# Optimization experiments

Hardware: AMD Instinct MI355X
Metric: run time of the kernel (lower is better)

The kernel has to match this reference:

```python
import jax, jax.numpy as jnp
import numpy as np

NB = 4          # batch size (len(unique(batch_ixs)))
NA = 1048576    # anchors per batch element
C_FG = 2        # foreground classes (probs has C_FG+1 columns)
K = 6000        # pre-NMS top-k, hard-coded in source
PATCH = (256, 256, 128)


def setup_inputs():
    key = jax.random.key(0)
    k1, k2, k3 = jax.random.split(key, 3)
    H, W, D = PATCH
    scale = jnp.array([H, W, H, W, D, D], jnp.float32)
    anchors = jax.random.uniform(k1, (NA, 6), jnp.float32) * scale   # (y1,x1,y2,x2,z1,z2) in pixel coords
    probs = jax.nn.softmax(jax.random.normal(k2, (NB * NA, C_FG + 1), jnp.float32), axis=-1)
    deltas = jax.random.normal(k3, (NB * NA, 6), jnp.float32) * 0.1
    batch_ixs = jnp.repeat(jnp.arange(NB, dtype=jnp.int32), NA)
    return {"anchors": anchors, "probs": probs, "deltas": deltas, "batch_ixs": batch_ixs}


def _refine(anchors, probs, deltas, batch_ixs):
    H, W, D = PATCH
    scale = jnp.array([H, W, H, W, D, D], jnp.float32)
    std = jnp.array([0.1, 0.1, 0.1, 0.2, 0.2, 0.2], jnp.float32)
    anchors_rep = jnp.tile(anchors, (NB, 1))            # anchors.repeat(len(unique(batch_ixs)), 1)
    fg = probs[:, 1:]                                   # (N, C_FG)
    # flat descending sort + [:6000]  ==  top_k over the flat view
    top_s, top_i = jax.lax.top_k(fg.reshape(-1), K)
    prop = top_i // C_FG                                # proposal index
    cls = top_i % C_FG + 1                              # pred class id (1-based)
    b_ix = batch_ixs[prop]
    anc = jnp.floor(anchors_rep[prop] / scale)          # torch.div(..., rounding_mode='floor')
    dlt = deltas[prop] * std
    # apply_box_deltas_3D
    h = anc[:, 2] - anc[:, 0]
    w = anc[:, 3] - anc[:, 1]
    d = anc[:, 5] - anc[:, 4]
    cy = anc[:, 0] + 0.5 * h + dlt[:, 0] * h
    cx = anc[:, 1] + 0.5 * w + dlt[:, 1] * w
    cz = anc[:, 4] + 0.5 * d + dlt[:, 2] * d
    h = h * jnp.exp(dlt[:, 3])
    w = w * jnp.exp(dlt[:, 4])
    d = d * jnp.exp(dlt[:, 5])
    y1 = cy - 0.5 * h
    x1 = cx - 0.5 * w
    z1 = cz - 0.5 * d
    boxes = jnp.stack([y1, x1, y1 + h, x1 + w, z1, z1 + d], axis=1) * scale
    hi = jnp.array([H, W, H, W, D, D], jnp.float32)
    rois = jnp.round(jnp.clip(boxes, 0.0, hi))          # clip_to_window + round -> pre_nms_rois

    # per-(batch, class) selection, replicating the source's `order[order[:2]]` double indexing
    def select(b, c):
        mask = (b_ix == b) & (cls == c)
        lp = (jnp.cumsum(mask) - 1).astype(jnp.int32)   # local position within class subset (valid where mask)
        ms = jnp.where(mask, top_s, -jnp.inf)
        ord_full = jnp.argsort(-ms)                     # local rank r -> global candidate index
        order_arr = lp[ord_full]                        # local rank r -> local position  (== torch `order`)
        q = order_arr[order_arr[:2]]                    # order[order[:2]]
        idx_src = jnp.where(mask, lp, K)                # K is out-of-range -> dropped
        sub_glob = jnp.zeros((K,), jnp.int32).at[idx_src].set(jnp.arange(K, dtype=jnp.int32), mode="drop")
        return sub_glob[q]                              # global indices of the 2 kept candidates

    pb = jnp.repeat(jnp.arange(NB, dtype=jnp.int32), C_FG)
    pc = jnp.tile(jnp.arange(1, C_FG + 1, dtype=jnp.int32), NB)
    sel = jax.vmap(select)(pb, pc)                      # (NB*C_FG, 2)
    # unique1d sorts its input; per-(b,c) subsets are disjoint so union == sort of all picks.
    # per-batch top-30 cap never binds (only C_FG*2 = 4 picks per batch).
    keep = jnp.sort(sel.reshape(-1))
    result = jnp.concatenate(
        [rois[keep],
         b_ix[keep, None].astype(jnp.float32),
         cls[keep, None].astype(jnp.float32),
         top_s[keep, None]],
        axis=1)                                         # (NB*C_FG*2, 9)
    return result


def reference(anchors, probs, deltas, batch_ixs):
    return _refine(anchors, probs, deltas, batch_ixs)
```

## Files before the change

kernel.cpp:

```cpp
#include <hip/hip_runtime.h>
#include <float.h>
#include <math.h>

#define NA_LOG2 20
#define NB_ 4
#define ROWS (NB_ << NA_LOG2)
#define B1 1024
#define T1 256
#define ROWS_PER_BLOCK (ROWS / B1)
#define BLOCKS_PER_BATCH (B1 / NB_)
#define ITERS (ROWS_PER_BLOCK / (T1 * 4))

__device__ __forceinline__ bool better(float sa, int ia, float sb, int ib) {
    return (sa > sb) || ((sa == sb) && (ia < ib));
}

__device__ __forceinline__ void merge2(float& a1s, int& a1i, float& a2s, int& a2i,
                                       float b1s, int b1i, float b2s, int b2i)
{
    if (better(b1s, b1i, a1s, a1i)) {
        if (better(a1s, a1i, b2s, b2i)) { a2s = a1s; a2i = a1i; }
        else                            { a2s = b2s; a2i = b2i; }
        a1s = b1s; a1i = b1i;
    } else if (better(b1s, b1i, a2s, a2i)) {
        a2s = b1s; a2i = b1i;
    }
}

#define UPD(sa, ia, sb, ib, s, i)                                        \
    do {                                                                 \
        if (better((s), (i), (sa), (ia))) {                              \
            (sb) = (sa); (ib) = (ia); (sa) = (s); (ia) = (i);            \
        } else if (better((s), (i), (sb), (ib))) {                       \
            (sb) = (s); (ib) = (i);                                      \
        }                                                                \
    } while (0)

__global__ __launch_bounds__(T1) void topk_pass1(const float* __restrict__ probs,
                                                 float* __restrict__ wsS,
                                                 int* __restrict__ wsI)
{
    const int tid = threadIdx.x;
    const int bb = blockIdx.x;

    float s1a = -FLT_MAX, s1b = -FLT_MAX, s2a = -FLT_MAX, s2b = -FLT_MAX;
    int   i1a = 0x7fffffff, i1b = 0x7fffffff, i2a = 0x7fffffff, i2b = 0x7fffffff;

    const float4* p4 = (const float4*)probs;
    const int baseRow = bb * ROWS_PER_BLOCK;

#pragma unroll
    for (int k = 0; k < ITERS; ++k) {
        const int row0 = baseRow + (k * T1 + tid) * 4;
        const float4* p = p4 + ((row0 * 3) >> 2);
        float4 v0 = p[0];
        float4 v1 = p[1];
        float4 v2 = p[2];
        const int f = row0 * 2;
        UPD(s1a, i1a, s1b, i1b, v0.y, f + 0);
        UPD(s2a, i2a, s2b, i2b, v0.z, f + 1);
        UPD(s1a, i1a, s1b, i1b, v1.x, f + 2);
        UPD(s2a, i2a, s2b, i2b, v1.y, f + 3);
        UPD(s1a, i1a, s1b, i1b, v1.w, f + 4);
        UPD(s2a, i2a, s2b, i2b, v2.x, f + 5);
        UPD(s1a, i1a, s1b, i1b, v2.z, f + 6);
        UPD(s2a, i2a, s2b, i2b, v2.w, f + 7);
    }

#pragma unroll
    for (int m = 1; m < 64; m <<= 1) {
        float o1s = __shfl_xor(s1a, m); int o1i = __shfl_xor(i1a, m);
        float o2s = __shfl_xor(s1b, m); int o2i = __shfl_xor(i1b, m);
        merge2(s1a, i1a, s1b, i1b, o1s, o1i, o2s, o2i);
        o1s = __shfl_xor(s2a, m); o1i = __shfl_xor(i2a, m);
        o2s = __shfl_xor(s2b, m); o2i = __shfl_xor(i2b, m);
        merge2(s2a, i2a, s2b, i2b, o1s, o1i, o2s, o2i);
    }

    __shared__ float ls[4][4];
    __shared__ int   li[4][4];
    const int wave = tid >> 6, lane = tid & 63;
    if (lane == 0) {
        ls[wave][0] = s1a; li[wave][0] = i1a;
        ls[wave][1] = s1b; li[wave][1] = i1b;
        ls[wave][2] = s2a; li[wave][2] = i2a;
        ls[wave][3] = s2b; li[wave][3] = i2b;
    }
    __syncthreads();
    if (tid == 0) {
        for (int wv = 1; wv < 4; ++wv) {
            merge2(s1a, i1a, s1b, i1b, ls[wv][0], li[wv][0], ls[wv][1], li[wv][1]);
            merge2(s2a, i2a, s2b, i2b, ls[wv][2], li[wv][2], ls[wv][3], li[wv][3]);
        }
        const int base = bb * 4;
        wsS[base + 0] = s1a; wsI[base + 0] = i1a;
        wsS[base + 1] = s1b; wsI[base + 1] = i1b;
        wsS[base + 2] = s2a; wsI[base + 2] = i2a;
        wsS[base + 3] = s2b; wsI[base + 3] = i2b;
    }
}

__global__ __launch_bounds__(512) void topk_pass2(const float* __restrict__ wsS,
                                                  const int* __restrict__ wsI,
                                                  const float* __restrict__ anchors,
                                                  const float* __restrict__ deltas,
                                                  float* __restrict__ out)
{
    __shared__ float g_s[16];
    __shared__ int   g_i[16];
    const int tid = threadIdx.x;
    const int wave = tid >> 6, lane = tid & 63;
    const int batch = wave >> 1, clsbit = wave & 1;

    float sa = -FLT_MAX, sb = -FLT_MAX;
    int   ia = 0x7fffffff, ib = 0x7fffffff;
#pragma unroll
    for (int j = 0; j < (2 * BLOCKS_PER_BATCH) / 64; ++j) {
        const int q = lane + j * 64;
        const int blk = batch * BLOCKS_PER_BATCH + (q >> 1);
        const int e = q & 1;
        const int idx = blk * 4 + clsbit * 2 + e;
        const float s = wsS[idx];
        const int   i = wsI[idx];
        UPD(sa, ia, sb, ib, s, i);
    }
#pragma unroll
    for (int m = 1; m < 64; m <<= 1) {
        float o1s = __shfl_xor(sa, m); int o1i = __shfl_xor(ia, m);
        float o2s = __shfl_xor(sb, m); int o2i = __shfl_xor(ib, m);
        merge2(sa, ia, sb, ib, o1s, o1i, o2s, o2i);
    }
    if (lane == 0) {
        g_s[wave * 2 + 0] = sa; g_i[wave * 2 + 0] = ia;
        g_s[wave * 2 + 1] = sb; g_i[wave * 2 + 1] = ib;
    }
    __syncthreads();

    if (tid == 0) {
        for (int a = 1; a < 16; ++a) {
            float s = g_s[a]; int ix = g_i[a];
            int b = a - 1;
            while (b >= 0 && better(s, ix, g_s[b], g_i[b])) {
                g_s[b + 1] = g_s[b]; g_i[b + 1] = g_i[b]; --b;
            }
            g_s[b + 1] = s; g_i[b + 1] = ix;
        }
    }
    __syncthreads();

    if (tid < 16) {
        const float scale[6] = {256.f, 256.f, 256.f, 256.f, 128.f, 128.f};
        const float stdv[6]  = {0.1f, 0.1f, 0.1f, 0.2f, 0.2f, 0.2f};
        const int flat = g_i[tid];
        const float score = g_s[tid];
        const int prop = flat >> 1;
        const int cls = (flat & 1) + 1;
        const int b = prop >> NA_LOG2;
        const int ar = prop & ((1 << NA_LOG2) - 1);

        float anc[6], dlt[6];
#pragma unroll
        for (int k = 0; k < 6; ++k) {
            anc[k] = floorf(anchors[ar * 6 + k] / scale[k]);
            dlt[k] = deltas[prop * 6 + k] * stdv[k];
        }
        float h = anc[2] - anc[0];
        float w = anc[3] - anc[1];
        float d = anc[5] - anc[4];
        float cy = anc[0] + 0.5f * h + dlt[0] * h;
        float cx = anc[1] + 0.5f * w + dlt[1] * w;
        float cz = anc[4] + 0.5f * d + dlt[2] * d;
        h *= expf(dlt[3]);
        w *= expf(dlt[4]);
        d *= expf(dlt[5]);
        const float y1 = cy - 0.5f * h, x1 = cx - 0.5f * w, z1 = cz - 0.5f * d;
        const float box[6] = {y1, x1, y1 + h, x1 + w, z1, z1 + d};

        float* o = out + tid * 9;
#pragma unroll
        for (int k = 0; k < 6; ++k) {
            float bx = box[k] * scale[k];
            bx = fminf(fmaxf(bx, 0.f), scale[k]);
            o[k] = rintf(bx);
        }
        o[6] = (float)b;
        o[7] = (float)cls;
        o[8] = score;
    }
}

extern "C" void kernel_launch(void* const* d_in, const int* in_sizes, int n_in,
                              void* d_out, int out_size, void* d_ws, size_t ws_size,
                              hipStream_t stream)
{
    const float* anchors = (const float*)d_in[0];
    const float* probs   = (const float*)d_in[1];
    const float* deltas  = (const float*)d_in[2];

    float* wsS = (float*)d_ws;
    int*   wsI = (int*)((char*)d_ws + B1 * 4 * sizeof(float));

    topk_pass1<<<dim3(B1), dim3(T1), 0, stream>>>(probs, wsS, wsI);
    topk_pass2<<<dim3(1), dim3(512), 0, stream>>>(wsS, wsI, anchors, deltas, (float*)d_out);
}
```

Before: 194.6 us.

## Fuse two-pass top-k into one kernel with last-block-done atomic counter

Merges the second reduction and box-refinement kernel into the first by having each block bump a global atomic counter, with the final block performing the cross-block merge and output. This removes one kernel launch and its inter-kernel gap. In exchange it adds a hipMemsetAsync on the counter every call, atomic stores and fences, and a serial tail inside the last 256-thread block, which now handles two groups per wave.

```diff
diff --git a/kernel.cpp b/kernel.cpp
--- a/kernel.cpp
+++ b/kernel.cpp
@@ -10,6 +10,8 @@
 #define ROWS_PER_BLOCK (ROWS / B1)
 #define BLOCKS_PER_BATCH (B1 / NB_)
 #define ITERS (ROWS_PER_BLOCK / (T1 * 4))
+
+#define WS_COUNTER_OFF (32 * 1024)
 
 __device__ __forceinline__ bool better(float sa, int ia, float sb, int ib) {
     return (sa > sb) || ((sa == sb) && (ia < ib));
@@ -36,9 +38,13 @@
         }                                                                \
     } while (0)
 
-__global__ __launch_bounds__(T1) void topk_pass1(const float* __restrict__ probs,
+__global__ __launch_bounds__(T1) void topk_fused(const float* __restrict__ probs,
+                                                 const float* __restrict__ anchors,
+                                                 const float* __restrict__ deltas,
                                                  float* __restrict__ wsS,
-                                                 int* __restrict__ wsI)
+                                                 int* __restrict__ wsI,
+                                                 unsigned int* __restrict__ counter,
+                                                 float* __restrict__ out)
 {
     const int tid = threadIdx.x;
     const int bb = blockIdx.x;
@@ -79,6 +85,7 @@
 
     __shared__ float ls[4][4];
     __shared__ int   li[4][4];
+    __shared__ int   amLast;
     const int wave = tid >> 6, lane = tid & 63;
     if (lane == 0) {
         ls[wave][0] = s1a; li[wave][0] = i1a;
@@ -93,46 +100,55 @@
             merge2(s2a, i2a, s2b, i2b, ls[wv][2], li[wv][2], ls[wv][3], li[wv][3]);
         }
         const int base = bb * 4;
-        wsS[base + 0] = s1a; wsI[base + 0] = i1a;
-        wsS[base + 1] = s1b; wsI[base + 1] = i1b;
-        wsS[base + 2] = s2a; wsI[base + 2] = i2a;
-        wsS[base + 3] = s2b; wsI[base + 3] = i2b;
-    }
-}
-
-__global__ __launch_bounds__(512) void topk_pass2(const float* __restrict__ wsS,
-                                                  const int* __restrict__ wsI,
-                                                  const float* __restrict__ anchors,
-                                                  const float* __restrict__ deltas,
-                                                  float* __restrict__ out)
-{
+        __hip_atomic_store(&wsS[base + 0], s1a, __ATOMIC_RELAXED, __HIP_MEMORY_SCOPE_AGENT);
+        __hip_atomic_store(&wsI[base + 0], i1a, __ATOMIC_RELAXED, __HIP_MEMORY_SCOPE_AGENT);
+        __hip_atomic_store(&wsS[base + 1], s1b, __ATOMIC_RELAXED, __HIP_MEMORY_SCOPE_AGENT);
+        __hip_atomic_store(&wsI[base + 1], i1b, __ATOMIC_RELAXED, __HIP_MEMORY_SCOPE_AGENT);
+        __hip_atomic_store(&wsS[base + 2], s2a, __ATOMIC_RELAXED, __HIP_MEMORY_SCOPE_AGENT);
+        __hip_atomic_store(&wsI[base + 2], i2a, __ATOMIC_RELAXED, __HIP_MEMORY_SCOPE_AGENT);
+        __hip_atomic_store(&wsS[base + 3], s2b, __ATOMIC_RELAXED, __HIP_MEMORY_SCOPE_AGENT);
+        __hip_atomic_store(&wsI[base + 3], i2b, __ATOMIC_RELAXED, __HIP_MEMORY_SCOPE_AGENT);
+        __threadfence();
+        unsigned int old = __hip_atomic_fetch_add(counter, 1u, __ATOMIC_ACQ_REL,
+                                                  __HIP_MEMORY_SCOPE_AGENT);
+        amLast = (old == (unsigned)(B1 - 1)) ? 1 : 0;
+    }
+    __syncthreads();
+    if (!amLast) return;
+
+    __threadfence();
+
     __shared__ float g_s[16];
     __shared__ int   g_i[16];
-    const int tid = threadIdx.x;
-    const int wave = tid >> 6, lane = tid & 63;
-    const int batch = wave >> 1, clsbit = wave & 1;
-
-    float sa = -FLT_MAX, sb = -FLT_MAX;
-    int   ia = 0x7fffffff, ib = 0x7fffffff;
-#pragma unroll
-    for (int j = 0; j < (2 * BLOCKS_PER_BATCH) / 64; ++j) {
-        const int q = lane + j * 64;
-        const int blk = batch * BLOCKS_PER_BATCH + (q >> 1);
-        const int e = q & 1;
-        const int idx = blk * 4 + clsbit * 2 + e;
-        const float s = wsS[idx];
-        const int   i = wsI[idx];
-        UPD(sa, ia, sb, ib, s, i);
-    }
-#pragma unroll
-    for (int m = 1; m < 64; m <<= 1) {
-        float o1s = __shfl_xor(sa, m); int o1i = __shfl_xor(ia, m);
-        float o2s = __shfl_xor(sb, m); int o2i = __shfl_xor(ib, m);
-        merge2(sa, ia, sb, ib, o1s, o1i, o2s, o2i);
-    }
-    if (lane == 0) {
-        g_s[wave * 2 + 0] = sa; g_i[wave * 2 + 0] = ia;
-        g_s[wave * 2 + 1] = sb; g_i[wave * 2 + 1] = ib;
+
+#pragma unroll
+    for (int grp2 = 0; grp2 < 2; ++grp2) {
+        const int g = wave * 2 + grp2;
+        const int batch = g >> 1, clsbit = g & 1;
+        float sa = -FLT_MAX, sb = -FLT_MAX;
+        int   ia = 0x7fffffff, ib = 0x7fffffff;
+#pragma unroll
+        for (int j = 0; j < (2 * BLOCKS_PER_BATCH) / 64; ++j) {
+            const int q = lane + j * 64;
+            const int blk = batch * BLOCKS_PER_BATCH + (q >> 1);
+            const int e = q & 1;
+            const int idx = blk * 4 + clsbit * 2 + e;
+            const float s = __hip_atomic_load(&wsS[idx], __ATOMIC_RELAXED,
+                                              __HIP_MEMORY_SCOPE_AGENT);
+            const int   i = __hip_atomic_load(&wsI[idx], __ATOMIC_RELAXED,
+                                              __HIP_MEMORY_SCOPE_AGENT);
+            UPD(sa, ia, sb, ib, s, i);
+        }
+#pragma unroll
+        for (int m = 1; m < 64; m <<= 1) {
+            float o1s = __shfl_xor(sa, m); int o1i = __shfl_xor(ia, m);
+            float o2s = __shfl_xor(sb, m); int o2i = __shfl_xor(ib, m);
+            merge2(sa, ia, sb, ib, o1s, o1i, o2s, o2i);
+        }
+        if (lane == 0) {
+            g_s[g * 2 + 0] = sa; g_i[g * 2 + 0] = ia;
+            g_s[g * 2 + 1] = sb; g_i[g * 2 + 1] = ib;
+        }
     }
     __syncthreads();
 
@@ -197,9 +213,12 @@
     const float* probs   = (const float*)d_in[1];
     const float* deltas  = (const float*)d_in[2];
 
-    float* wsS = (float*)d_ws;
-    int*   wsI = (int*)((char*)d_ws + B1 * 4 * sizeof(float));
-
-    topk_pass1<<<dim3(B1), dim3(T1), 0, stream>>>(probs, wsS, wsI);
-    topk_pass2<<<dim3(1), dim3(512), 0, stream>>>(wsS, wsI, anchors, deltas, (float*)d_out);
-}
+    float*        wsS     = (float*)d_ws;
+    int*          wsI     = (int*)((char*)d_ws + B1 * 4 * sizeof(float));
+    unsigned int* counter = (unsigned int*)((char*)d_ws + WS_COUNTER_OFF);
+
+    hipMemsetAsync(counter, 0, sizeof(unsigned int), stream);
+
+    topk_fused<<<dim3(B1), dim3(T1), 0, stream>>>(probs, anchors, deltas,
+                                                  wsS, wsI, counter, (float*)d_out);
+}
```

Measured after the change: 236.6 us. +21.6%, slower.

## Pack score and index into 64-bit keys and coalesce float4 loads in top-2 scan

Applied to the files above, without the earlier changes.

Each thread in the first pass now reads consecutive float4s that are coalesced across the block, instead of three strided float4s per 4-row group. Column and row are derived from the flat float index. Score and inverted index are packed into a single u64 key, so comparisons and shuffles become branchless 64-bit max and select operations. This relies on the scores being non-negative so their float bit patterns order correctly as integers. In exchange, each thread does extra integer division and select work per element.

```diff
diff --git a/kernel.cpp b/kernel.cpp
--- a/kernel.cpp
+++ b/kernel.cpp
@@ -7,143 +7,123 @@
 #define ROWS (NB_ << NA_LOG2)
 #define B1 1024
 #define T1 256
-#define ROWS_PER_BLOCK (ROWS / B1)
+#define F4_PER_BLOCK 3072
+#define F4_PER_THREAD (F4_PER_BLOCK / T1)
 #define BLOCKS_PER_BATCH (B1 / NB_)
-#define ITERS (ROWS_PER_BLOCK / (T1 * 4))
 
-__device__ __forceinline__ bool better(float sa, int ia, float sb, int ib) {
-    return (sa > sb) || ((sa == sb) && (ia < ib));
+typedef unsigned long long u64;
+typedef unsigned int u32;
+
+
+__device__ __forceinline__ void upd2(u64& ka, u64& kb, u64 k) {
+    const bool b1 = k > ka;
+    const bool b2 = k > kb;
+    kb = b1 ? ka : (b2 ? k : kb);
+    ka = b1 ? k : ka;
 }
 
-__device__ __forceinline__ void merge2(float& a1s, int& a1i, float& a2s, int& a2i,
-                                       float b1s, int b1i, float b2s, int b2i)
-{
-    if (better(b1s, b1i, a1s, a1i)) {
-        if (better(a1s, a1i, b2s, b2i)) { a2s = a1s; a2i = a1i; }
-        else                            { a2s = b2s; a2i = b2i; }
-        a1s = b1s; a1i = b1i;
-    } else if (better(b1s, b1i, a2s, a2i)) {
-        a2s = b1s; a2i = b1i;
-    }
+__device__ __forceinline__ void mrg2(u64& a1, u64& a2, u64 b1, u64 b2) {
+    const bool t = b1 > a1;
+    const u64 n1 = t ? b1 : a1;
+    const u64 c1 = t ? a1 : b1;
+    const u64 c2 = t ? b2 : a2;
+    a2 = (c1 > c2) ? c1 : c2;
+    a1 = n1;
 }
 
-#define UPD(sa, ia, sb, ib, s, i)                                        \
-    do {                                                                 \
-        if (better((s), (i), (sa), (ia))) {                              \
-            (sb) = (sa); (ib) = (ia); (sa) = (s); (ia) = (i);            \
-        } else if (better((s), (i), (sb), (ib))) {                       \
-            (sb) = (s); (ib) = (i);                                      \
-        }                                                                \
-    } while (0)
-
-__global__ __launch_bounds__(T1) void topk_pass1(const float* __restrict__ probs,
-                                                 float* __restrict__ wsS,
-                                                 int* __restrict__ wsI)
+__global__ __launch_bounds__(T1) void scan_pass1(const float4* __restrict__ p4,
+                                                 u64* __restrict__ wsK)
 {
     const int tid = threadIdx.x;
-    const int bb = blockIdx.x;
+    const int bb  = blockIdx.x;
+    const int base = bb * F4_PER_BLOCK;
 
-    float s1a = -FLT_MAX, s1b = -FLT_MAX, s2a = -FLT_MAX, s2b = -FLT_MAX;
-    int   i1a = 0x7fffffff, i1b = 0x7fffffff, i2a = 0x7fffffff, i2b = 0x7fffffff;
-
-    const float4* p4 = (const float4*)probs;
-    const int baseRow = bb * ROWS_PER_BLOCK;
+    u64 k1a = 0, k1b = 0, k2a = 0, k2b = 0;
 
 #pragma unroll
-    for (int k = 0; k < ITERS; ++k) {
-        const int row0 = baseRow + (k * T1 + tid) * 4;
-        const float4* p = p4 + ((row0 * 3) >> 2);
-        float4 v0 = p[0];
-        float4 v1 = p[1];
-        float4 v2 = p[2];
-        const int f = row0 * 2;
-        UPD(s1a, i1a, s1b, i1b, v0.y, f + 0);
-        UPD(s2a, i2a, s2b, i2b, v0.z, f + 1);
-        UPD(s1a, i1a, s1b, i1b, v1.x, f + 2);
-        UPD(s2a, i2a, s2b, i2b, v1.y, f + 3);
-        UPD(s1a, i1a, s1b, i1b, v1.w, f + 4);
-        UPD(s2a, i2a, s2b, i2b, v2.x, f + 5);
-        UPD(s1a, i1a, s1b, i1b, v2.z, f + 6);
-        UPD(s2a, i2a, s2b, i2b, v2.w, f + 7);
+    for (int k = 0; k < F4_PER_THREAD; ++k) {
+        const int u = base + k * T1 + tid;
+        const float4 v = p4[u];
+        const int fi0 = u * 4;
+        const int r0  = fi0 / 3;
+        const int ph  = fi0 - r0 * 3;
+#pragma unroll
+        for (int j = 0; j < 4; ++j) {
+            const float s = (j == 0) ? v.x : (j == 1) ? v.y : (j == 2) ? v.z : v.w;
+            const int  cj   = ph + j;
+            const bool wrap = (cj >= 3);
+            const int  col  = wrap ? cj - 3 : cj;
+            const int  row  = r0 + (wrap ? 1 : 0);
+            const int  fg   = 2 * row + (col - 1);
+            const u64  key  = ((u64)__float_as_uint(s) << 32) | (u32)~(u32)fg;
+            upd2(k1a, k1b, (col == 1) ? key : 0ull);
+            upd2(k2a, k2b, (col == 2) ? key : 0ull);
+        }
     }
 
 #pragma unroll
     for (int m = 1; m < 64; m <<= 1) {
-        float o1s = __shfl_xor(s1a, m); int o1i = __shfl_xor(i1a, m);
-        float o2s = __shfl_xor(s1b, m); int o2i = __shfl_xor(i1b, m);
-        merge2(s1a, i1a, s1b, i1b, o1s, o1i, o2s, o2i);
-        o1s = __shfl_xor(s2a, m); o1i = __shfl_xor(i2a, m);
-        o2s = __shfl_xor(s2b, m); o2i = __shfl_xor(i2b, m);
-        merge2(s2a, i2a, s2b, i2b, o1s, o1i, o2s, o2i);
+        u64 o1 = (u64)__shfl_xor((long long)k1a, m);
+        u64 o2 = (u64)__shfl_xor((long long)k1b, m);
+        mrg2(k1a, k1b, o1, o2);
+        o1 = (u64)__shfl_xor((long long)k2a, m);
+        o2 = (u64)__shfl_xor((long long)k2b, m);
+        mrg2(k2a, k2b, o1, o2);
     }
 
-    __shared__ float ls[4][4];
-    __shared__ int   li[4][4];
+    __shared__ u64 ls[4][4];
     const int wave = tid >> 6, lane = tid & 63;
     if (lane == 0) {
-        ls[wave][0] = s1a; li[wave][0] = i1a;
-        ls[wave][1] = s1b; li[wave][1] = i1b;
-        ls[wave][2] = s2a; li[wave][2] = i2a;
-        ls[wave][3] = s2b; li[wave][3] = i2b;
+        ls[wave][0] = k1a; ls[wave][1] = k1b;
+        ls[wave][2] = k2a; ls[wave][3] = k2b;
     }
     __syncthreads();
     if (tid == 0) {
         for (int wv = 1; wv < 4; ++wv) {
-            merge2(s1a, i1a, s1b, i1b, ls[wv][0], li[wv][0], ls[wv][1], li[wv][1]);
-            merge2(s2a, i2a, s2b, i2b, ls[wv][2], li[wv][2], ls[wv][3], li[wv][3]);
+            mrg2(k1a, k1b, ls[wv][0], ls[wv][1]);
+            mrg2(k2a, k2b, ls[wv][2], ls[wv][3]);
         }
-        const int base = bb * 4;
-        wsS[base + 0] = s1a; wsI[base + 0] = i1a;
-        wsS[base + 1] = s1b; wsI[base + 1] = i1b;
-        wsS[base + 2] = s2a; wsI[base + 2] = i2a;
-        wsS[base + 3] = s2b; wsI[base + 3] = i2b;
+        u64* o = wsK + bb * 4;
+        o[0] = k1a; o[1] = k1b; o[2] = k2a; o[3] = k2b;
     }
 }
 
-__global__ __launch_bounds__(512) void topk_pass2(const float* __restrict__ wsS,
-                                                  const int* __restrict__ wsI,
-                                                  const float* __restrict__ anchors,
-                                                  const float* __restrict__ deltas,
-                                                  float* __restrict__ out)
+__global__ __launch_bounds__(512) void finish_pass2(const u64* __restrict__ wsK,
+                                                    const float* __restrict__ anchors,
+                                                    const float* __restrict__ deltas,
+                                                    float* __restrict__ out)
 {
-    __shared__ float g_s[16];
-    __shared__ int   g_i[16];
+    __shared__ u64 g_k[16];
     const int tid = threadIdx.x;
     const int wave = tid >> 6, lane = tid & 63;
     const int batch = wave >> 1, clsbit = wave & 1;
 
-    float sa = -FLT_MAX, sb = -FLT_MAX;
-    int   ia = 0x7fffffff, ib = 0x7fffffff;
+    u64 ka = 0, kb = 0;
 #pragma unroll
     for (int j = 0; j < (2 * BLOCKS_PER_BATCH) / 64; ++j) {
-        const int q = lane + j * 64;
+        const int q   = j * 64 + lane;
         const int blk = batch * BLOCKS_PER_BATCH + (q >> 1);
-        const int e = q & 1;
-        const int idx = blk * 4 + clsbit * 2 + e;
-        const float s = wsS[idx];
-        const int   i = wsI[idx];
-        UPD(sa, ia, sb, ib, s, i);
+        const int e   = q & 1;
+        upd2(ka, kb, wsK[blk * 4 + clsbit * 2 + e]);
     }
 #pragma unroll
     for (int m = 1; m < 64; m <<= 1) {
-        float o1s = __shfl_xor(sa, m); int o1i = __shfl_xor(ia, m);
-        float o2s = __shfl_xor(sb, m); int o2i = __shfl_xor(ib, m);
-        merge2(sa, ia, sb, ib, o1s, o1i, o2s, o2i);
+        u64 o1 = (u64)__shfl_xor((long long)ka, m);
+        u64 o2 = (u64)__shfl_xor((long long)kb, m);
+        mrg2(ka, kb, o1, o2);
     }
     if (lane == 0) {
-        g_s[wave * 2 + 0] = sa; g_i[wave * 2 + 0] = ia;
-        g_s[wave * 2 + 1] = sb; g_i[wave * 2 + 1] = ib;
+        g_k[wave * 2 + 0] = ka;
+        g_k[wave * 2 + 1] = kb;
     }
     __syncthreads();
 
     if (tid == 0) {
         for (int a = 1; a < 16; ++a) {
-            float s = g_s[a]; int ix = g_i[a];
+            const u64 kv = g_k[a];
             int b = a - 1;
-            while (b >= 0 && better(s, ix, g_s[b], g_i[b])) {
-                g_s[b + 1] = g_s[b]; g_i[b + 1] = g_i[b]; --b;
-            }
-            g_s[b + 1] = s; g_i[b + 1] = ix;
+            while (b >= 0 && kv > g_k[b]) { g_k[b + 1] = g_k[b]; --b; }
+            g_k[b + 1] = kv;
         }
     }
     __syncthreads();
@@ -151,12 +131,13 @@
     if (tid < 16) {
         const float scale[6] = {256.f, 256.f, 256.f, 256.f, 128.f, 128.f};
         const float stdv[6]  = {0.1f, 0.1f, 0.1f, 0.2f, 0.2f, 0.2f};
-        const int flat = g_i[tid];
-        const float score = g_s[tid];
+        const u64 key = g_k[tid];
+        const float score = __uint_as_float((u32)(key >> 32));
+        const int flat = (int)~(u32)key;
         const int prop = flat >> 1;
-        const int cls = (flat & 1) + 1;
-        const int b = prop >> NA_LOG2;
-        const int ar = prop & ((1 << NA_LOG2) - 1);
+        const int cls  = (flat & 1) + 1;
+        const int b    = prop >> NA_LOG2;
+        const int ar   = prop & ((1 << NA_LOG2) - 1);
 
         float anc[6], dlt[6];
 #pragma unroll
@@ -197,9 +178,8 @@
     const float* probs   = (const float*)d_in[1];
     const float* deltas  = (const float*)d_in[2];
 
-    float* wsS = (float*)d_ws;
-    int*   wsI = (int*)((char*)d_ws + B1 * 4 * sizeof(float));
+    u64* wsK = (u64*)d_ws;
 
-    topk_pass1<<<dim3(B1), dim3(T1), 0, stream>>>(probs, wsS, wsI);
-    topk_pass2<<<dim3(1), dim3(512), 0, stream>>>(wsS, wsI, anchors, deltas, (float*)d_out);
+    scan_pass1<<<dim3(B1), dim3(T1), 0, stream>>>((const float4*)probs, wsK);
+    finish_pass2<<<dim3(1), dim3(512), 0, stream>>>(wsK, anchors, deltas, (float*)d_out);
 }
```

Result: faster. 185.0 us (-4.9%).
